# Performance work log

Hardware: AMD Instinct MI355X
Metric: run time of the kernel (lower is better)

The kernel has to match this reference:

```python
import jax, jax.numpy as jnp
import numpy as np
from jax import lax

DIM, DIN, NST, DTR, K = 96, 192, 16, 6, 4
B, H, W = 2, 56, 56
MID, SEMID = 24, 24
EPS = 1e-5


def _ln(x, g, b):
    m = x.mean(-1, keepdims=True)
    v = ((x - m) ** 2).mean(-1, keepdims=True)
    return (x - m) / jnp.sqrt(v + EPS) * g + b


def _bn(x, g, b, m, v):  # eval-mode BatchNorm2d, NCHW
    return (x - m[None, :, None, None]) / jnp.sqrt(v[None, :, None, None] + EPS) * g[None, :, None, None] + b[None, :, None, None]


def _conv(x, w, pad, groups=1):
    return lax.conv_general_dilated(x, w, (1, 1), [(pad, pad), (pad, pad)],
                                    dimension_numbers=('NCHW', 'OIHW', 'NCHW'),
                                    feature_group_count=groups)


def _vssm(xn, in_proj_w, conv_w, conv_b, x_proj_w, dt_proj_w, dt_proj_b,
          A_log, Ds, out_norm_g, out_norm_b, out_proj_w):
    Bz, Hh, Ww, C = xn.shape
    L = Hh * Ww
    xz = xn @ in_proj_w.T                      # (B,H,W,2*Din)
    xc, z = jnp.split(xz, 2, axis=-1)
    xc = xc.transpose(0, 3, 1, 2)              # (B,Din,H,W)
    xc = _conv(xc, conv_w, pad=1, groups=DIN) + conv_b[None, :, None, None]
    xc = jax.nn.silu(xc)
    # 4 scan directions: row-major, col-major, and their reverses
    x1 = xc.reshape(Bz, DIN, L)
    x2 = xc.transpose(0, 1, 3, 2).reshape(Bz, DIN, L)
    xs = jnp.stack([x1, x2], axis=1)
    xs = jnp.concatenate([xs, jnp.flip(xs, axis=-1)], axis=1)   # (B,4,Din,L)
    x_dbl = jnp.einsum('bkdl,kcd->bkcl', xs, x_proj_w)          # (B,4,dtR+2N,L)
    dts, Bs, Cs = jnp.split(x_dbl, [DTR, DTR + NST], axis=2)
    delta = jax.nn.softplus(jnp.einsum('bkrl,kdr->bkdl', dts, dt_proj_w)
                            + dt_proj_b[None, :, :, None])      # (B,4,Din,L)
    A = -jnp.exp(A_log).reshape(K, DIN, NST)
    dA = jnp.exp(jnp.einsum('bkdl,kdn->bkdln', delta, A))       # (B,4,Din,L,N)
    dBu = jnp.einsum('bkdl,bknl,bkdl->bkdln', delta, Bs, xs)

    def comb(c1, c2):
        a1, b1 = c1
        a2, b2 = c2
        return (a1 * a2, a2 * b1 + b2)

    _, hs = lax.associative_scan(comb, (dA, dBu), axis=3)       # h_t = dA_t h_{t-1} + dBu_t
    ys = jnp.einsum('bkdln,bknl->bkdl', hs, Cs) + Ds.reshape(1, K, DIN, 1) * xs
    inv = jnp.flip(ys[:, 2:4], axis=-1)

    def t_back(y):
        return y.reshape(Bz, DIN, Ww, Hh).transpose(0, 1, 3, 2).reshape(Bz, DIN, L)

    y = ys[:, 0] + t_back(ys[:, 1]) + inv[:, 0] + t_back(inv[:, 1])
    y = y.reshape(Bz, DIN, Hh, Ww).transpose(0, 2, 3, 1)        # (B,H,W,Din)
    y = _ln(y, out_norm_g, out_norm_b) * jax.nn.silu(z)
    return y @ out_proj_w.T                                      # (B,H,W,dim)


def setup_inputs() -> dict:
    key = jax.random.key(0)
    ks = jax.random.split(key, 16)
    r = lambda k, s, sc=0.05: (jax.random.normal(k, s, dtype=jnp.float32) * sc)
    d = {}
    d['x'] = jax.random.normal(ks[0], (B, DIM, H, W), dtype=jnp.float32)
    d['norm1_g'] = jnp.ones((DIM,), jnp.float32); d['norm1_b'] = jnp.zeros((DIM,), jnp.float32)
    d['in_proj_w'] = r(ks[1], (2 * DIN, DIM))
    d['conv_w'] = r(ks[2], (DIN, 1, 3, 3), 0.2); d['conv_b'] = jnp.zeros((DIN,), jnp.float32)
    d['x_proj_w'] = r(ks[3], (K, DTR + 2 * NST, DIN))
    d['dt_proj_w'] = r(ks[4], (K, DIN, DTR), 0.2)
    d['dt_proj_b'] = jnp.full((K, DIN), -2.0, jnp.float32)
    d['A_log'] = jnp.log(jnp.broadcast_to(jnp.arange(1, NST + 1, dtype=jnp.float32), (K * DIN, NST)) + 0.0)
    d['Ds'] = jnp.ones((K * DIN,), jnp.float32)
    d['out_norm_g'] = jnp.ones((DIN,), jnp.float32); d['out_norm_b'] = jnp.zeros((DIN,), jnp.float32)
    d['out_proj_w'] = r(ks[5], (DIM, DIN))
    d['scale1'] = jnp.full((DIM,), 0.1, jnp.float32)
    d['norm2_g'] = jnp.ones((DIM,), jnp.float32); d['norm2_b'] = jnp.zeros((DIM,), jnp.float32)
    d['lc_w1'] = r(ks[6], (MID, DIM, 1, 1), 0.1)
    d['lc_g1'] = jnp.ones((MID,), jnp.float32); d['lc_b1'] = jnp.zeros((MID,), jnp.float32)
    d['lc_m1'] = jnp.zeros((MID,), jnp.float32); d['lc_v1'] = jnp.ones((MID,), jnp.float32)
    d['lc_w2'] = r(ks[7], (MID, MID, 3, 3), 0.1)
    d['lc_g2'] = jnp.ones((MID,), jnp.float32); d['lc_b2'] = jnp.zeros((MID,), jnp.float32)
    d['lc_m2'] = jnp.zeros((MID,), jnp.float32); d['lc_v2'] = jnp.ones((MID,), jnp.float32)
    d['lc_w3'] = r(ks[8], (DIM, MID, 1, 1), 0.1)
    d['lc_g3'] = jnp.ones((DIM,), jnp.float32); d['lc_b3'] = jnp.zeros((DIM,), jnp.float32)
    d['lc_m3'] = jnp.zeros((DIM,), jnp.float32); d['lc_v3'] = jnp.ones((DIM,), jnp.float32)
    d['se_w1'] = r(ks[9], (SEMID, DIM), 0.1)
    d['se_w2'] = r(ks[10], (DIM, SEMID), 0.1)
    d['scale2'] = jnp.full((DIM,), 0.1, jnp.float32)
    return d


def reference(x, norm1_g, norm1_b, in_proj_w, conv_w, conv_b, x_proj_w, dt_proj_w,
              dt_proj_b, A_log, Ds, out_norm_g, out_norm_b, out_proj_w, scale1,
              norm2_g, norm2_b, lc_w1, lc_g1, lc_b1, lc_m1, lc_v1, lc_w2, lc_g2,
              lc_b2, lc_m2, lc_v2, lc_w3, lc_g3, lc_b3, lc_m3, lc_v3, se_w1,
              se_w2, scale2):
    x_hwc = x.transpose(0, 2, 3, 1)                    # (B,H,W,C)
    vl = _vssm(_ln(x_hwc, norm1_g, norm1_b), in_proj_w, conv_w, conv_b,
               x_proj_w, dt_proj_w, dt_proj_b, A_log, Ds,
               out_norm_g, out_norm_b, out_proj_w)
    vl = vl + scale1 * x_hwc                           # scaled residual
    vb = _ln(vl, norm2_g, norm2_b).transpose(0, 3, 1, 2)  # (B,C,H,W)
    h = jax.nn.relu(_bn(_conv(vb, lc_w1, pad=0), lc_g1, lc_b1, lc_m1, lc_v1))
    h = jax.nn.relu(_bn(_conv(h, lc_w2, pad=1), lc_g2, lc_b2, lc_m2, lc_v2))
    h = _bn(_conv(h, lc_w3, pad=0), lc_g3, lc_b3, lc_m3, lc_v3)
    # SE channel attention
    w = h.mean(axis=(2, 3))                            # (B,C)
    w = jax.nn.sigmoid(jax.nn.relu(w @ se_w1.T) @ se_w2.T)
    h = h * w[:, :, None, None]
    return h + scale2[None, :, None, None] * vl.transpose(0, 3, 1, 2)
```

## Files before the change

### kernel.cpp

```cpp
#include <hip/hip_runtime.h>
#include <math.h>

#define DIMC 96
#define DINC 192
#define NSTC 16
#define DTRC 6
#define KDIR 4
#define BB   2
#define HH   56
#define WWD  56
#define LL   3136
#define NPIX (BB*LL)
#define EPSF 1e-5f
#define NCH  98
#define LC   32
#define NCHAIN (BB*KDIR*DINC)
#define NCOLS 152

#define OFF_XCRAW  0u
#define OFF_XCONV  1204224u
#define OFF_ZS     2408448u
#define OFF_DTS    3612672u
#define OFF_BCB    3763200u
#define OFF_BCC    4164608u
#define OFF_XSCANT 4566016u
#define OFF_CUMD   9382912u
#define OFF_YS     14199808u
#define OFF_HENDT  0u
#define OFF_SUMDT  19016704u
#define OFF_VL     9382912u
#define OFF_H1     9985024u
#define OFF_H2     10135552u
#define OFF_H3     10286080u
#define OFF_POOL   10888192u
#define OFF_SEW    10888384u

__device__ __forceinline__ float siluf(float x) { return x / (1.f + __expf(-x)); }
__device__ __forceinline__ float softplusf(float x) {
    return fmaxf(x, 0.f) + __logf(1.f + __expf(-fabsf(x)));
}
__device__ __forceinline__ float fexp2(float x) {
#if __has_builtin(__builtin_amdgcn_exp2f)
    return __builtin_amdgcn_exp2f(x);
#else
    return exp2f(x);
#endif
}
#define LOG2E 1.44269504088896f

__global__ __launch_bounds__(256) void gemm1_k(const float* __restrict__ x,
                                               const float* __restrict__ g,
                                               const float* __restrict__ bt,
                                               const float* __restrict__ W,
                                               float* __restrict__ xcr,
                                               float* __restrict__ zs) {
    __shared__ float xT[64 * 97];
    __shared__ float wT[96 * 100];
    __shared__ float mA[64], iA[64];
    int row0 = blockIdx.x * 64;
    int b = row0 / LL, pos0 = row0 % LL;
    int c0 = blockIdx.y * 96;
    for (int f = threadIdx.x; f < 96 * 16; f += 256) {
        int ch = f >> 4, po = (f & 15) * 4;
        float4 v = *(const float4*)&x[((size_t)b * DIMC + ch) * LL + pos0 + po];
        xT[(po + 0) * 97 + ch] = v.x; xT[(po + 1) * 97 + ch] = v.y;
        xT[(po + 2) * 97 + ch] = v.z; xT[(po + 3) * 97 + ch] = v.w;
    }
    for (int f = threadIdx.x; f < 96 * 24; f += 256) {
        int r = f / 24, kq = (f % 24) * 4;
        *(float4*)&wT[r * 100 + kq] = *(const float4*)&W[(size_t)(c0 + r) * DIMC + kq];
    }
    __syncthreads();
    if (threadIdx.x < 64) {
        float s = 0.f, q = 0.f;
        const float* xr = &xT[threadIdx.x * 97];
        for (int c = 0; c < 96; ++c) { float v = xr[c]; s += v; q = fmaf(v, v, q); }
        float m = s * (1.f / 96.f);
        mA[threadIdx.x] = m;
        iA[threadIdx.x] = rsqrtf(q * (1.f / 96.f) - m * m + EPSF);
    }
    __syncthreads();
    for (int e = threadIdx.x; e < 64 * 96; e += 256) {
        int row = e / 96, col = e - row * 96;
        float v = xT[row * 97 + col];
        xT[row * 97 + col] = (v - mA[row]) * iA[row] * g[col] + bt[col];
    }
    __syncthreads();
    int tc = threadIdx.x & 15, tr = threadIdx.x >> 4;
    float acc[4][6] = {};
    for (int k = 0; k < 96; ++k) {
        float xv[4], wv[6];
#pragma unroll
        for (int i = 0; i < 4; ++i) xv[i] = xT[(4 * tr + i) * 97 + k];
#pragma unroll
        for (int j = 0; j < 6; ++j) wv[j] = wT[(tc + 16 * j) * 100 + k];
#pragma unroll
        for (int i = 0; i < 4; ++i)
#pragma unroll
            for (int j = 0; j < 6; ++j) acc[i][j] = fmaf(xv[i], wv[j], acc[i][j]);
    }
    int pos = pos0 + 4 * tr;
    if (c0 < DINC) {
#pragma unroll
        for (int j = 0; j < 6; ++j) {
            int col = c0 + tc + 16 * j;
            float4 v = make_float4(acc[0][j], acc[1][j], acc[2][j], acc[3][j]);
            *(float4*)&xcr[((size_t)b * DINC + col) * LL + pos] = v;
        }
    } else {
#pragma unroll
        for (int i = 0; i < 4; ++i)
#pragma unroll
            for (int j = 0; j < 6; ++j) {
                int zc = c0 - DINC + tc + 16 * j;
                zs[(size_t)(row0 + 4 * tr + i) * DINC + zc] = siluf(acc[i][j]);
            }
    }
}

__global__ __launch_bounds__(448) void dwconv_k(const float* __restrict__ xcr,
                                                const float* __restrict__ cw,
                                                const float* __restrict__ cb,
                                                float* __restrict__ xconv) {
    __shared__ float P[56 * 57];
    int bd = blockIdx.x;
    int d = bd % DINC;
    size_t base = (size_t)bd * LL;
    for (int t = threadIdx.x; t < LL; t += 448)
        P[(t / 56) * 57 + (t % 56)] = xcr[base + t];
    float wk[9];
#pragma unroll
    for (int q = 0; q < 9; ++q) wk[q] = cw[d * 9 + q];
    float bias = cb[d];
    __syncthreads();
    for (int t = threadIdx.x; t < LL; t += 448) {
        int h = t / 56, w = t % 56;
        float acc = bias;
#pragma unroll
        for (int ky = 0; ky < 3; ++ky) {
            int y = h + ky - 1;
            if ((unsigned)y >= 56u) continue;
#pragma unroll
            for (int kx = 0; kx < 3; ++kx) {
                int xq = w + kx - 1;
                if ((unsigned)xq >= 56u) continue;
                acc = fmaf(wk[ky * 3 + kx], P[y * 57 + xq], acc);
            }
        }
        xconv[base + t] = siluf(acc);
    }
}

__global__ __launch_bounds__(256) void gemmx_k(const float* __restrict__ xconv,
                                               const float* __restrict__ xpw,
                                               float* __restrict__ dts,
                                               float* __restrict__ bcB,
                                               float* __restrict__ bcC,
                                               float* __restrict__ xscanT) {
    __shared__ float xT[64 * 49];
    __shared__ float wT[NCOLS * 52];
    int row0 = blockIdx.x * 64;
    int b = row0 / LL, pos0 = row0 % LL;
    int tc = threadIdx.x & 15, tr = threadIdx.x >> 4;
    float acc[4][10] = {};
    for (int kc = 0; kc < 4; ++kc) {
        if (kc) __syncthreads();
        for (int f = threadIdx.x; f < 48 * 16; f += 256) {
            int dd = f >> 4, po = (f & 15) * 4;
            float4 v = *(const float4*)&xconv[((size_t)b * DINC + kc * 48 + dd) * LL + pos0 + po];
            xT[(po + 0) * 49 + dd] = v.x; xT[(po + 1) * 49 + dd] = v.y;
            xT[(po + 2) * 49 + dd] = v.z; xT[(po + 3) * 49 + dd] = v.w;
        }
        for (int f = threadIdx.x; f < NCOLS * 12; f += 256) {
            int r = f / 12, kq = (f % 12) * 4;
            *(float4*)&wT[r * 52 + kq] = *(const float4*)&xpw[(size_t)r * DINC + kc * 48 + kq];
        }
        __syncthreads();
        for (int k = 0; k < 48; ++k) {
            float xv[4], wv[10];
#pragma unroll
            for (int i = 0; i < 4; ++i) xv[i] = xT[(4 * tr + i) * 49 + k];
#pragma unroll
            for (int j = 0; j < 10; ++j) {
                int c = tc + 16 * j;
                wv[j] = (c < NCOLS) ? wT[c * 52 + k] : 0.f;
            }
#pragma unroll
            for (int i = 0; i < 4; ++i)
#pragma unroll
                for (int j = 0; j < 10; ++j) acc[i][j] = fmaf(xv[i], wv[j], acc[i][j]);
        }
        for (int f = threadIdx.x; f < 64 * 48; f += 256) {
            int i = f / 48, dd = f - 48 * (f / 48);
            float v = xT[i * 49 + dd];
            int pos = pos0 + i;
            int hh = pos / 56, w = pos - 56 * hh;
            int lt = w * 56 + hh;
            size_t bb = (size_t)b * KDIR;
            int col = kc * 48 + dd;
            xscanT[((bb + 0) * LL + pos) * DINC + col] = v;
            xscanT[((bb + 1) * LL + lt) * DINC + col] = v;
            xscanT[((bb + 2) * LL + (LL - 1 - pos)) * DINC + col] = v;
            xscanT[((bb + 3) * LL + (LL - 1 - lt)) * DINC + col] = v;
        }
    }
#pragma unroll
    for (int i = 0; i < 4; ++i) {
        int pos = pos0 + 4 * tr + i;
        int h = pos / 56, w = pos - 56 * h;
        int lt = w * 56 + h;
#pragma unroll
        for (int j = 0; j < 10; ++j) {
            int c = tc + 16 * j;
            if (c >= NCOLS) continue;
            int k = c / 38, idx = c - 38 * k;
            int l = (k == 0) ? pos : (k == 1) ? lt : (k == 2) ? (LL - 1 - pos) : (LL - 1 - lt);
            size_t rb = (size_t)(b * KDIR + k) * LL + l;
            float v = acc[i][j];
            if (idx < DTRC)    dts[rb * DTRC + idx] = v;
            else if (idx < 22) bcB[rb * NSTC + (idx - 6)] = v;
            else               bcC[rb * NSTC + (idx - 22)] = v;
        }
    }
}

__global__ __launch_bounds__(64) void pass1_k(const float* __restrict__ dts,
                                              const float* __restrict__ bcB,
                                              const float* __restrict__ bcC,
                                              const float* __restrict__ alog,
                                              const float* __restrict__ dtw,
                                              const float* __restrict__ dtb,
                                              const float* __restrict__ xscanT,
                                              float* __restrict__ hendT,
                                              float* __restrict__ sumdT,
                                              float* __restrict__ ysT,
                                              float* __restrict__ cumdT) {
    __shared__ float sdt[LC * 7];
    __shared__ float sB[LC * 16];
    __shared__ float sC[LC * 16];
    int blk = blockIdx.x;
    int c = blk % NCH;
    int dtile = (blk / NCH) % 3;
    int bk = blk / (NCH * 3);
    int k = bk & 3;
    int l0 = c * LC;
    int t = threadIdx.x;
    int d = dtile * 64 + t;
    const float* dsrc = dts + ((size_t)bk * LL + l0) * DTRC;
    for (int f = t; f < LC * DTRC; f += 64) sdt[(f / DTRC) * 7 + (f % DTRC)] = dsrc[f];
    const float* bB = bcB + ((size_t)bk * LL + l0) * NSTC;
    const float* bC = bcC + ((size_t)bk * LL + l0) * NSTC;
    for (int f = t; f < LC * NSTC; f += 64) { sB[f] = bB[f]; sC[f] = bC[f]; }
    float wr[DTRC];
    {
        const float* wp = dtw + ((size_t)k * DINC + d) * DTRC;
#pragma unroll
        for (int r = 0; r < DTRC; ++r) wr[r] = wp[r];
    }
    float bias = dtb[k * DINC + d];
    float An2[NSTC];
    {
        const float* ap = alog + ((size_t)(k * DINC + d)) * NSTC;
#pragma unroll
        for (int n = 0; n < NSTC; ++n) An2[n] = -__expf(ap[n]) * LOG2E;
    }
    __syncthreads();
    float h[NSTC];
#pragma unroll
    for (int n = 0; n < NSTC; ++n) h[n] = 0.f;
    float cum = 0.f;
    const float* xrow = xscanT + ((size_t)bk * LL + l0) * DINC + d;
    float* yrow = ysT + ((size_t)bk * LL + l0) * DINC + d;
    float* crow = cumdT + ((size_t)bk * LL + l0) * DINC + d;
#pragma unroll 8
    for (int s = 0; s < LC; ++s) {
        float acc = bias;
#pragma unroll
        for (int r = 0; r < DTRC; ++r) acc = fmaf(wr[r], sdt[s * 7 + r], acc);
        float dv = softplusf(acc);
        float xv = xrow[(size_t)s * DINC];
        cum += dv;
        float dx = dv * xv;
        const float4* B4 = (const float4*)&sB[s * 16];
        const float4* C4 = (const float4*)&sC[s * 16];
        float y = 0.f;
#pragma unroll
        for (int nq = 0; nq < 4; ++nq) {
            float4 Bv = B4[nq], Cv = C4[nq];
            float e0 = fexp2(An2[nq * 4 + 0] * dv);
            h[nq * 4 + 0] = fmaf(e0, h[nq * 4 + 0], dx * Bv.x);
            y = fmaf(h[nq * 4 + 0], Cv.x, y);
            float e1 = fexp2(An2[nq * 4 + 1] * dv);
            h[nq * 4 + 1] = fmaf(e1, h[nq * 4 + 1], dx * Bv.y);
            y = fmaf(h[nq * 4 + 1], Cv.y, y);
            float e2 = fexp2(An2[nq * 4 + 2] * dv);
            h[nq * 4 + 2] = fmaf(e2, h[nq * 4 + 2], dx * Bv.z);
            y = fmaf(h[nq * 4 + 2], Cv.z, y);
            float e3 = fexp2(An2[nq * 4 + 3] * dv);
            h[nq * 4 + 3] = fmaf(e3, h[nq * 4 + 3], dx * Bv.w);
            y = fmaf(h[nq * 4 + 3], Cv.w, y);
        }
        yrow[(size_t)s * DINC] = y;
        crow[(size_t)s * DINC] = cum;
    }
#pragma unroll
    for (int n = 0; n < NSTC; ++n)
        hendT[((size_t)(bk * NCH + c) * NSTC + n) * DINC + d] = h[n];
    sumdT[(size_t)(bk * NCH + c) * DINC + d] = cum;
}

__global__ __launch_bounds__(256) void scan2_k(float* __restrict__ hendT,
                                               const float* __restrict__ sumdT,
                                               const float* __restrict__ alog) {
    int gid = blockIdx.x * 256 + threadIdx.x;
    int d = gid % DINC;
    int n = (gid / DINC) % NSTC;
    int bk = gid / (DINC * NSTC);
    int k = bk & 3;
    float An2 = -__expf(alog[((size_t)(k * DINC + d)) * NSTC + n]) * LOG2E;
    float h = 0.f;
#pragma unroll 4
    for (int c = 0; c < NCH; ++c) {
        size_t idx = ((size_t)(bk * NCH + c) * NSTC + n) * DINC + d;
        float he = hendT[idx];
        float sd = sumdT[(size_t)(bk * NCH + c) * DINC + d];
        hendT[idx] = h;
        h = fmaf(fexp2(An2 * sd), h, he);
    }
}

__global__ __launch_bounds__(256) void pass2_k(const float* __restrict__ bcC,
                                               const float* __restrict__ alog,
                                               const float* __restrict__ hpreT,
                                               const float* __restrict__ cumdT,
                                               float* __restrict__ ysT) {
    __shared__ float sA2[DINC * 17];
    __shared__ float sH[DINC * 17];
    __shared__ float sC[LC * NSTC];
    int blk = blockIdx.x;
    int c = blk % NCH;
    int bk = blk / NCH;
    int k = bk & 3;
    int l0 = c * LC;
    int tid = threadIdx.x;
    const float* ap = alog + (size_t)k * DINC * NSTC;
    for (int f = tid; f < DINC * NSTC; f += 256) {
        int dq = f / NSTC, n = f % NSTC;
        sA2[dq * 17 + n] = -__expf(ap[f]) * LOG2E;
    }
    for (int f = tid; f < DINC * NSTC; f += 256) {
        int n = f / DINC, dq = f % DINC;
        sH[dq * 17 + n] = hpreT[((size_t)(bk * NCH + c) * NSTC + n) * DINC + dq];
    }
    const float* bC = bcC + ((size_t)bk * LL + l0) * NSTC;
    for (int f = tid; f < LC * NSTC; f += 256) sC[f] = bC[f];
    __syncthreads();
    for (int e = tid; e < LC * DINC; e += 256) {
        int li = e / DINC, d = e - DINC * (e / DINC);
        size_t gq = ((size_t)bk * LL + l0 + li) * DINC + d;
        float cd = cumdT[gq];
        float y = ysT[gq];
        const float* A = &sA2[d * 17];
        const float* Hp = &sH[d * 17];
        const float* Cp = &sC[li * NSTC];
#pragma unroll
        for (int n = 0; n < NSTC; ++n)
            y = fmaf(Hp[n] * fexp2(A[n] * cd), Cp[n], y);
        ysT[gq] = y;
    }
}

__global__ __launch_bounds__(256) void gemm2_k(const float* __restrict__ ysT,
                                               const float* __restrict__ xscanT,
                                               const float* __restrict__ dsv,
                                               const float* __restrict__ g,
                                               const float* __restrict__ bt,
                                               const float* __restrict__ zs,
                                               const float* __restrict__ opw,
                                               const float* __restrict__ x,
                                               const float* __restrict__ sc1,
                                               float* __restrict__ vl) {
    __shared__ float xT[64 * 193];
    __shared__ float wT[96 * 52];
    __shared__ float mA[64], iA[64];
    __shared__ float sD[DINC];
    int row0 = blockIdx.x * 64;
    int b = row0 / LL, pos0 = row0 % LL;
    if (threadIdx.x < DINC)
        sD[threadIdx.x] = dsv[threadIdx.x] + dsv[DINC + threadIdx.x] +
                          dsv[2 * DINC + threadIdx.x] + dsv[3 * DINC + threadIdx.x];
    __syncthreads();
    size_t base = (size_t)b * KDIR * LL;
    for (int f = threadIdx.x; f < 64 * DINC; f += 256) {
        int r = f / DINC, d = f - DINC * (f / DINC);
        int pos = pos0 + r;
        int hh = pos / 56, w = pos - 56 * hh;
        int lt = w * 56 + hh;
        float y = ysT[(base + pos) * DINC + d]
                + ysT[(base + LL + lt) * DINC + d]
                + ysT[(base + 2 * LL + (LL - 1 - pos)) * DINC + d]
                + ysT[(base + 3 * LL + (LL - 1 - lt)) * DINC + d];
        float xv = xscanT[(base + pos) * DINC + d];
        xT[r * 193 + d] = fmaf(xv, sD[d], y);
    }
    __syncthreads();
    if (threadIdx.x < 64) {
        float s = 0.f, q = 0.f;
        const float* xr = &xT[threadIdx.x * 193];
        for (int c = 0; c < 192; ++c) { float v = xr[c]; s += v; q = fmaf(v, v, q); }
        float m = s * (1.f / 192.f);
        mA[threadIdx.x] = m;
        iA[threadIdx.x] = rsqrtf(q * (1.f / 192.f) - m * m + EPSF);
    }
    __syncthreads();
    for (int e = threadIdx.x; e < 64 * 192; e += 256) {
        int row = e / 192, col = e - row * 192;
        float v = xT[row * 193 + col];
        float z = zs[(size_t)row0 * DINC + e];
        xT[row * 193 + col] = ((v - mA[row]) * iA[row] * g[col] + bt[col]) * z;
    }
    int tc = threadIdx.x & 15, tr = threadIdx.x >> 4;
    float acc[4][6] = {};
    for (int kc = 0; kc < 4; ++kc) {
        __syncthreads();
        for (int f = threadIdx.x; f < 96 * 12; f += 256) {
            int r = f / 12, kq = (f % 12) * 4;
            *(float4*)&wT[r * 52 + kq] = *(const float4*)&opw[(size_t)r * DINC + kc * 48 + kq];
        }
        __syncthreads();
        for (int k = 0; k < 48; ++k) {
            float xv[4], wv[6];
#pragma unroll
            for (int i = 0; i < 4; ++i) xv[i] = xT[(4 * tr + i) * 193 + kc * 48 + k];
#pragma unroll
            for (int j = 0; j < 6; ++j) wv[j] = wT[(tc + 16 * j) * 52 + k];
#pragma unroll
            for (int i = 0; i < 4; ++i)
#pragma unroll
                for (int j = 0; j < 6; ++j) acc[i][j] = fmaf(xv[i], wv[j], acc[i][j]);
        }
    }
#pragma unroll
    for (int i = 0; i < 4; ++i) {
        int pos = pos0 + 4 * tr + i;
#pragma unroll
        for (int j = 0; j < 6; ++j) {
            int col = tc + 16 * j;
            float v = fmaf(sc1[col], x[((size_t)b * DIMC + col) * LL + pos], acc[i][j]);
            vl[(size_t)(row0 + 4 * tr + i) * DIMC + col] = v;
        }
    }
}

__global__ __launch_bounds__(256) void ln2conv1_k(const float* __restrict__ vl,
                                                  const float* __restrict__ g,
                                                  const float* __restrict__ bt,
                                                  const float* __restrict__ w1,
                                                  const float* __restrict__ g1,
                                                  const float* __restrict__ b1,
                                                  const float* __restrict__ m1,
                                                  const float* __restrict__ v1,
                                                  float* __restrict__ h1) {
    __shared__ float row[4][96];
    int wv = threadIdx.x >> 6, lane = threadIdx.x & 63;
    int pix = blockIdx.x * 4 + wv;
    const float* vr = vl + (size_t)pix * DIMC;
    float a0 = vr[lane];
    float a1 = (lane < 32) ? vr[64 + lane] : 0.f;
    float s = a0 + a1, q = a0 * a0 + a1 * a1;
    for (int o = 32; o; o >>= 1) { s += __shfl_xor(s, o, 64); q += __shfl_xor(q, o, 64); }
    float m = s * (1.f / 96.f);
    float inv = rsqrtf(q * (1.f / 96.f) - m * m + EPSF);
    row[wv][lane] = (a0 - m) * inv * g[lane] + bt[lane];
    if (lane < 32) row[wv][64 + lane] = (a1 - m) * inv * g[64 + lane] + bt[64 + lane];
    __syncthreads();
    if (lane < 24) {
        const float* wr = w1 + lane * 96;
        float acc = 0.f;
#pragma unroll 8
        for (int c = 0; c < 96; ++c) acc = fmaf(row[wv][c], wr[c], acc);
        float bn = (acc - m1[lane]) * rsqrtf(v1[lane] + EPSF) * g1[lane] + b1[lane];
        int b = pix / LL, pos = pix % LL;
        h1[((size_t)b * 24 + lane) * LL + pos] = fmaxf(bn, 0.f);
    }
}

__global__ __launch_bounds__(256) void conv2_k(const float* __restrict__ h1,
                                               const float* __restrict__ w2,
                                               const float* __restrict__ g2,
                                               const float* __restrict__ b2,
                                               const float* __restrict__ m2,
                                               const float* __restrict__ v2,
                                               float* __restrict__ h2) {
    int i = blockIdx.x * 256 + threadIdx.x;
    int pos = i % LL, mo = (i / LL) % 24, b = i / (LL * 24);
    int hh = pos / WWD, ww = pos % WWD;
    float acc = 0.f;
    for (int c = 0; c < 24; ++c) {
        const float* src = h1 + ((size_t)b * 24 + c) * LL;
        const float* wk = w2 + ((size_t)(mo * 24 + c)) * 9;
#pragma unroll
        for (int ky = 0; ky < 3; ++ky) {
            int y = hh + ky - 1;
            if ((unsigned)y >= HH) continue;
#pragma unroll
            for (int kx = 0; kx < 3; ++kx) {
                int xq = ww + kx - 1;
                if ((unsigned)xq >= WWD) continue;
                acc = fmaf(wk[ky * 3 + kx], src[y * WWD + xq], acc);
            }
        }
    }
    float bn = (acc - m2[mo]) * rsqrtf(v2[mo] + EPSF) * g2[mo] + b2[mo];
    h2[i] = fmaxf(bn, 0.f);
}

__global__ __launch_bounds__(256) void conv3_k(const float* __restrict__ h2,
                                               const float* __restrict__ w3,
                                               const float* __restrict__ g3,
                                               const float* __restrict__ b3,
                                               const float* __restrict__ m3,
                                               const float* __restrict__ v3,
                                               float* __restrict__ h3) {
    int i = blockIdx.x * 256 + threadIdx.x;
    int pos = i % LL, c = (i / LL) % DIMC, b = i / (LL * DIMC);
    const float* wr = w3 + c * 24;
    float acc = 0.f;
#pragma unroll
    for (int mo = 0; mo < 24; ++mo)
        acc = fmaf(wr[mo], h2[((size_t)b * 24 + mo) * LL + pos], acc);
    h3[i] = (acc - m3[c]) * rsqrtf(v3[c] + EPSF) * g3[c] + b3[c];
}

__global__ __launch_bounds__(256) void pool_k(const float* __restrict__ h3,
                                              float* __restrict__ pooled) {
    int bc = blockIdx.x;
    const float* p = h3 + (size_t)bc * LL;
    float s = 0.f;
    for (int i = threadIdx.x; i < LL; i += 256) s += p[i];
    for (int o = 32; o; o >>= 1) s += __shfl_xor(s, o, 64);
    __shared__ float wsum[4];
    if ((threadIdx.x & 63) == 0) wsum[threadIdx.x >> 6] = s;
    __syncthreads();
    if (threadIdx.x == 0) pooled[bc] = (wsum[0] + wsum[1] + wsum[2] + wsum[3]) * (1.f / 3136.f);
}

__global__ __launch_bounds__(128) void semlp_k(const float* __restrict__ pooled,
                                               const float* __restrict__ sw1,
                                               const float* __restrict__ sw2,
                                               float* __restrict__ sew) {
    __shared__ float pl[2][96];
    __shared__ float hid[2][24];
    for (int i = threadIdx.x; i < 192; i += 128) pl[i / 96][i % 96] = pooled[i];
    __syncthreads();
    if (threadIdx.x < 48) {
        int b = threadIdx.x / 24, mo = threadIdx.x % 24;
        float acc = 0.f;
        for (int c = 0; c < 96; ++c) acc = fmaf(pl[b][c], sw1[mo * 96 + c], acc);
        hid[b][mo] = fmaxf(acc, 0.f);
    }
    __syncthreads();
    for (int i = threadIdx.x; i < 192; i += 128) {
        int b = i / 96, c = i % 96;
        float acc = 0.f;
        for (int mo = 0; mo < 24; ++mo) acc = fmaf(hid[b][mo], sw2[c * 24 + mo], acc);
        sew[i] = 1.f / (1.f + __expf(-acc));
    }
}

__global__ __launch_bounds__(256) void final_k(const float* __restrict__ h3,
                                               const float* __restrict__ sew,
                                               const float* __restrict__ vl,
                                               const float* __restrict__ sc2,
                                               float* __restrict__ out) {
    int i = blockIdx.x * 256 + threadIdx.x;
    int pos = i % LL, c = (i / LL) % DIMC, b = i / (LL * DIMC);
    out[i] = fmaf(h3[i], sew[b * DIMC + c],
                  sc2[c] * vl[((size_t)b * LL + pos) * DIMC + c]);
}

extern "C" void kernel_launch(void* const* d_in, const int* in_sizes, int n_in,
                              void* d_out, int out_size, void* d_ws, size_t ws_size,
                              hipStream_t stream) {
    const float* x    = (const float*)d_in[0];
    const float* n1g  = (const float*)d_in[1];
    const float* n1b  = (const float*)d_in[2];
    const float* ipw  = (const float*)d_in[3];
    const float* cw   = (const float*)d_in[4];
    const float* cb   = (const float*)d_in[5];
    const float* xpw  = (const float*)d_in[6];
    const float* dtw  = (const float*)d_in[7];
    const float* dtb  = (const float*)d_in[8];
    const float* alog = (const float*)d_in[9];
    const float* dsv  = (const float*)d_in[10];
    const float* ong  = (const float*)d_in[11];
    const float* onb  = (const float*)d_in[12];
    const float* opw  = (const float*)d_in[13];
    const float* sc1  = (const float*)d_in[14];
    const float* n2g  = (const float*)d_in[15];
    const float* n2b  = (const float*)d_in[16];
    const float* w1   = (const float*)d_in[17];
    const float* g1   = (const float*)d_in[18];
    const float* b1   = (const float*)d_in[19];
    const float* m1   = (const float*)d_in[20];
    const float* v1   = (const float*)d_in[21];
    const float* w2   = (const float*)d_in[22];
    const float* g2   = (const float*)d_in[23];
    const float* b2   = (const float*)d_in[24];
    const float* m2   = (const float*)d_in[25];
    const float* v2   = (const float*)d_in[26];
    const float* w3   = (const float*)d_in[27];
    const float* g3   = (const float*)d_in[28];
    const float* b3   = (const float*)d_in[29];
    const float* m3   = (const float*)d_in[30];
    const float* v3   = (const float*)d_in[31];
    const float* sw1  = (const float*)d_in[32];
    const float* sw2  = (const float*)d_in[33];
    const float* sc2  = (const float*)d_in[34];
    float* ws = (float*)d_ws;
    float* out = (float*)d_out;

    gemm1_k<<<dim3(NPIX / 64, 4), 256, 0, stream>>>(x, n1g, n1b, ipw,
                                                    ws + OFF_XCRAW, ws + OFF_ZS);
    dwconv_k<<<BB * DINC, 448, 0, stream>>>(ws + OFF_XCRAW, cw, cb, ws + OFF_XCONV);
    gemmx_k<<<NPIX / 64, 256, 0, stream>>>(ws + OFF_XCONV, xpw, ws + OFF_DTS,
                                           ws + OFF_BCB, ws + OFF_BCC, ws + OFF_XSCANT);

    pass1_k<<<BB * KDIR * 3 * NCH, 64, 0, stream>>>(
        ws + OFF_DTS, ws + OFF_BCB, ws + OFF_BCC, alog, dtw, dtb,
        ws + OFF_XSCANT, ws + OFF_HENDT, ws + OFF_SUMDT, ws + OFF_YS, ws + OFF_CUMD);
    scan2_k<<<(NCHAIN * NSTC) / 256, 256, 0, stream>>>(ws + OFF_HENDT, ws + OFF_SUMDT, alog);
    pass2_k<<<BB * KDIR * NCH, 256, 0, stream>>>(
        ws + OFF_BCC, alog, ws + OFF_HENDT, ws + OFF_CUMD, ws + OFF_YS);

    gemm2_k<<<NPIX / 64, 256, 0, stream>>>(ws + OFF_YS, ws + OFF_XSCANT, dsv,
                                           ong, onb, ws + OFF_ZS, opw, x, sc1, ws + OFF_VL);
    ln2conv1_k<<<NPIX / 4, 256, 0, stream>>>(ws + OFF_VL, n2g, n2b, w1, g1, b1, m1, v1,
                                             ws + OFF_H1);
    conv2_k<<<(BB * 24 * LL) / 256, 256, 0, stream>>>(ws + OFF_H1, w2, g2, b2, m2, v2,
                                                      ws + OFF_H2);
    conv3_k<<<(BB * DIMC * LL) / 256, 256, 0, stream>>>(ws + OFF_H2, w3, g3, b3, m3, v3,
                                                        ws + OFF_H3);
    pool_k<<<BB * DIMC, 256, 0, stream>>>(ws + OFF_H3, ws + OFF_POOL);
    semlp_k<<<1, 128, 0, stream>>>(ws + OFF_POOL, sw1, sw2, ws + OFF_SEW);
    final_k<<<(BB * DIMC * LL) / 256, 256, 0, stream>>>(ws + OFF_H3, ws + OFF_SEW, ws + OFF_VL,
                                                        sc2, out);
    (void)in_sizes; (void)n_in; (void)out_size; (void)ws_size;
}
```

Before: 252.3 us.

## Store only two scan-direction copies of x and shrink gemmx row tile

```diff
diff --git a/kernel.cpp b/kernel.cpp
--- a/kernel.cpp
+++ b/kernel.cpp
@@ -24,16 +24,16 @@
 #define OFF_BCB    3763200u
 #define OFF_BCC    4164608u
 #define OFF_XSCANT 4566016u
-#define OFF_CUMD   9382912u
-#define OFF_YS     14199808u
+#define OFF_CUMD   6974464u
+#define OFF_YS     11791360u
 #define OFF_HENDT  0u
-#define OFF_SUMDT  19016704u
-#define OFF_VL     9382912u
-#define OFF_H1     9985024u
-#define OFF_H2     10135552u
-#define OFF_H3     10286080u
-#define OFF_POOL   10888192u
-#define OFF_SEW    10888384u
+#define OFF_SUMDT  16608256u
+#define OFF_VL     6974464u
+#define OFF_H1     7576576u
+#define OFF_H2     7727104u
+#define OFF_H3     7877632u
+#define OFF_POOL   8479744u
+#define OFF_SEW    8479936u
 
 __device__ __forceinline__ float siluf(float x) { return x / (1.f + __expf(-x)); }
 __device__ __forceinline__ float softplusf(float x) {
@@ -157,16 +157,16 @@
                                                float* __restrict__ bcB,
                                                float* __restrict__ bcC,
                                                float* __restrict__ xscanT) {
-    __shared__ float xT[64 * 49];
+    __shared__ float xT[16 * 49];
     __shared__ float wT[NCOLS * 52];
-    int row0 = blockIdx.x * 64;
+    int row0 = blockIdx.x * 16;
     int b = row0 / LL, pos0 = row0 % LL;
     int tc = threadIdx.x & 15, tr = threadIdx.x >> 4;
-    float acc[4][10] = {};
+    float acc[10] = {};
     for (int kc = 0; kc < 4; ++kc) {
         if (kc) __syncthreads();
-        for (int f = threadIdx.x; f < 48 * 16; f += 256) {
-            int dd = f >> 4, po = (f & 15) * 4;
+        for (int f = threadIdx.x; f < 48 * 4; f += 256) {
+            int dd = f >> 2, po = (f & 3) * 4;
             float4 v = *(const float4*)&xconv[((size_t)b * DINC + kc * 48 + dd) * LL + pos0 + po];
             xT[(po + 0) * 49 + dd] = v.x; xT[(po + 1) * 49 + dd] = v.y;
             xT[(po + 2) * 49 + dd] = v.z; xT[(po + 3) * 49 + dd] = v.w;
@@ -176,37 +176,32 @@
             *(float4*)&wT[r * 52 + kq] = *(const float4*)&xpw[(size_t)r * DINC + kc * 48 + kq];
         }
         __syncthreads();
+#pragma unroll 4
         for (int k = 0; k < 48; ++k) {
-            float xv[4], wv[10];
-#pragma unroll
-            for (int i = 0; i < 4; ++i) xv[i] = xT[(4 * tr + i) * 49 + k];
+            float xv = xT[tr * 49 + k];
+            float wv[10];
 #pragma unroll
             for (int j = 0; j < 10; ++j) {
                 int c = tc + 16 * j;
                 wv[j] = (c < NCOLS) ? wT[c * 52 + k] : 0.f;
             }
 #pragma unroll
-            for (int i = 0; i < 4; ++i)
-#pragma unroll
-                for (int j = 0; j < 10; ++j) acc[i][j] = fmaf(xv[i], wv[j], acc[i][j]);
-        }
-        for (int f = threadIdx.x; f < 64 * 48; f += 256) {
+            for (int j = 0; j < 10; ++j) acc[j] = fmaf(xv, wv[j], acc[j]);
+        }
+        for (int f = threadIdx.x; f < 16 * 48; f += 256) {
             int i = f / 48, dd = f - 48 * (f / 48);
             float v = xT[i * 49 + dd];
             int pos = pos0 + i;
             int hh = pos / 56, w = pos - 56 * hh;
             int lt = w * 56 + hh;
-            size_t bb = (size_t)b * KDIR;
+            size_t bb = (size_t)b * 2;
             int col = kc * 48 + dd;
             xscanT[((bb + 0) * LL + pos) * DINC + col] = v;
             xscanT[((bb + 1) * LL + lt) * DINC + col] = v;
-            xscanT[((bb + 2) * LL + (LL - 1 - pos)) * DINC + col] = v;
-            xscanT[((bb + 3) * LL + (LL - 1 - lt)) * DINC + col] = v;
-        }
-    }
-#pragma unroll
-    for (int i = 0; i < 4; ++i) {
-        int pos = pos0 + 4 * tr + i;
+        }
+    }
+    {
+        int pos = pos0 + tr;
         int h = pos / 56, w = pos - 56 * h;
         int lt = w * 56 + h;
 #pragma unroll
@@ -216,7 +211,7 @@
             int k = c / 38, idx = c - 38 * k;
             int l = (k == 0) ? pos : (k == 1) ? lt : (k == 2) ? (LL - 1 - pos) : (LL - 1 - lt);
             size_t rb = (size_t)(b * KDIR + k) * LL + l;
-            float v = acc[i][j];
+            float v = acc[j];
             if (idx < DTRC)    dts[rb * DTRC + idx] = v;
             else if (idx < 22) bcB[rb * NSTC + (idx - 6)] = v;
             else               bcC[rb * NSTC + (idx - 22)] = v;
@@ -242,7 +237,7 @@
     int c = blk % NCH;
     int dtile = (blk / NCH) % 3;
     int bk = blk / (NCH * 3);
-    int k = bk & 3;
+    int k = bk & 3, b = bk >> 2;
     int l0 = c * LC;
     int t = threadIdx.x;
     int d = dtile * 64 + t;
@@ -269,7 +264,9 @@
 #pragma unroll
     for (int n = 0; n < NSTC; ++n) h[n] = 0.f;
     float cum = 0.f;
-    const float* xrow = xscanT + ((size_t)bk * LL + l0) * DINC + d;
+    bool rev = (k >= 2);
+    const float* xbase = xscanT + ((size_t)(b * 2 + (k & 1)) * LL) * DINC + d;
+    int xi0 = rev ? (LL - 1 - l0) : l0;
     float* yrow = ysT + ((size_t)bk * LL + l0) * DINC + d;
     float* crow = cumdT + ((size_t)bk * LL + l0) * DINC + d;
 #pragma unroll 8
@@ -278,7 +275,7 @@
 #pragma unroll
         for (int r = 0; r < DTRC; ++r) acc = fmaf(wr[r], sdt[s * 7 + r], acc);
         float dv = softplusf(acc);
-        float xv = xrow[(size_t)s * DINC];
+        float xv = xbase[(size_t)(rev ? (xi0 - s) : (xi0 + s)) * DINC];
         cum += dv;
         float dx = dv * xv;
         const float4* B4 = (const float4*)&sB[s * 16];
@@ -391,6 +388,7 @@
                           dsv[2 * DINC + threadIdx.x] + dsv[3 * DINC + threadIdx.x];
     __syncthreads();
     size_t base = (size_t)b * KDIR * LL;
+    size_t xbase = (size_t)b * 2 * LL;
     for (int f = threadIdx.x; f < 64 * DINC; f += 256) {
         int r = f / DINC, d = f - DINC * (f / DINC);
         int pos = pos0 + r;
@@ -400,7 +398,7 @@
                 + ysT[(base + LL + lt) * DINC + d]
                 + ysT[(base + 2 * LL + (LL - 1 - pos)) * DINC + d]
                 + ysT[(base + 3 * LL + (LL - 1 - lt)) * DINC + d];
-        float xv = xscanT[(base + pos) * DINC + d];
+        float xv = xscanT[(xbase + pos) * DINC + d];
         xT[r * 193 + d] = fmaf(xv, sD[d], y);
     }
     __syncthreads();
@@ -623,7 +621,7 @@
     gemm1_k<<<dim3(NPIX / 64, 4), 256, 0, stream>>>(x, n1g, n1b, ipw,
                                                     ws + OFF_XCRAW, ws + OFF_ZS);
     dwconv_k<<<BB * DINC, 448, 0, stream>>>(ws + OFF_XCRAW, cw, cb, ws + OFF_XCONV);
-    gemmx_k<<<NPIX / 64, 256, 0, stream>>>(ws + OFF_XCONV, xpw, ws + OFF_DTS,
+    gemmx_k<<<NPIX / 16, 256, 0, stream>>>(ws + OFF_XCONV, xpw, ws + OFF_DTS,
                                            ws + OFF_BCB, ws + OFF_BCC, ws + OFF_XSCANT);
 
     pass1_k<<<BB * KDIR * 3 * NCH, 64, 0, stream>>>(
```

New measurement: 244.1 us. 3.2% less time.
